# Kernel optimization log

Hardware: AMD Instinct MI355X
Metric: run time of the kernel (lower is better)

The kernel has to match this reference:

```python
import jax, jax.numpy as jnp
import numpy as np

D_MODEL = 1024
DFF = 4096
SPARSITY = 0.5
EPS = 1e-6


def layer_norm(x, gamma, beta):
    mu = jnp.mean(x, axis=-1, keepdims=True)
    var = jnp.mean(jnp.square(x - mu), axis=-1, keepdims=True)
    return (x - mu) * jax.lax.rsqrt(var + EPS) * gamma + beta


def setup_inputs() -> dict:
    key = jax.random.key(0)
    ks = jax.random.split(key, 8)
    B, S, d, f = 4, 2048, D_MODEL, DFF
    s = 1.0 / np.sqrt(d)
    return {
        "x": jax.random.normal(ks[0], (B, S, d), dtype=jnp.float32),
        "Wq": jax.random.normal(ks[1], (d, d), dtype=jnp.float32) * s,
        "bq": jnp.zeros((d,), jnp.float32),
        "Wk": jax.random.normal(ks[2], (d, d), dtype=jnp.float32) * s,
        "bk": jnp.zeros((d,), jnp.float32),
        "Wv": jax.random.normal(ks[3], (d, d), dtype=jnp.float32) * s,
        "bv": jnp.zeros((d,), jnp.float32),
        "W1": jax.random.normal(ks[4], (d, f), dtype=jnp.float32) * s,
        "b1": jnp.zeros((f,), jnp.float32),
        "W2": jax.random.normal(ks[5], (f, d), dtype=jnp.float32) * (1.0 / np.sqrt(f)),
        "b2": jnp.zeros((d,), jnp.float32),
        "gamma1": jnp.ones((d,), jnp.float32),
        "beta1": jnp.zeros((d,), jnp.float32),
        "gamma2": jnp.ones((d,), jnp.float32),
        "beta2": jnp.zeros((d,), jnp.float32),
    }


def reference(x, Wq, bq, Wk, bk, Wv, bv, W1, b1, W2, b2, gamma1, beta1, gamma2, beta2):
    B, S, d = x.shape
    q = x @ Wq + bq
    k = x @ Wk + bk
    v = x @ Wv + bv
    # scores: [B, S, S], scaled by sqrt(d_model)
    scores = jnp.einsum("bqd,bkd->bqk", q, k) / jnp.sqrt(jnp.float32(d))
    # top-k sparsification: keep scores >= row-wise k-th largest, else 0
    topk = int(SPARSITY * S)
    top_vals = jax.lax.top_k(scores, topk)[0]  # sorted descending
    threshold = top_vals[..., -1:]
    sparse_scores = jnp.where(scores >= threshold, scores, jnp.zeros_like(scores))
    attn = jax.nn.softmax(sparse_scores, axis=-1)
    attn_out = jnp.einsum("bqk,bkd->bqd", attn, v)
    out1 = layer_norm(x + attn_out, gamma1, beta1)
    ffn = jax.nn.relu(out1 @ W1 + b1) @ W2 + b2
    return layer_norm(out1 + ffn, gamma2, beta2)
```

## Files before the change

kernel.cpp:

```cpp
#include <hip/hip_runtime.h>
#include <cstdint>

typedef unsigned short u16;
typedef __attribute__((ext_vector_type(8))) short s16x8;
typedef __attribute__((ext_vector_type(4))) unsigned short u16x4;
typedef __attribute__((ext_vector_type(4))) float f32x4;

__device__ __forceinline__ u16 f2bf(float f) {
  union { float f; uint32_t u; } c; c.f = f;
  uint32_t r = c.u + 0x7FFFu + ((c.u >> 16) & 1u);
  return (u16)(r >> 16);
}
__device__ __forceinline__ float wave_sum_f(float v) {
#pragma unroll
  for (int o = 32; o > 0; o >>= 1) v += __shfl_xor(v, o);
  return v;
}
__device__ __forceinline__ float wave_max_f(float v) {
#pragma unroll
  for (int o = 32; o > 0; o >>= 1) v = fmaxf(v, __shfl_xor(v, o));
  return v;
}
__device__ __forceinline__ void gload16(const u16* g, u16* l) {
  __builtin_amdgcn_global_load_lds(
      (const __attribute__((address_space(1))) unsigned int*)g,
      (__attribute__((address_space(3))) unsigned int*)l,
      16, 0, 0);
}

__global__ __launch_bounds__(256)
void cast_f32_bf16(const float* __restrict__ in, u16* __restrict__ out) {
  long i = ((long)blockIdx.x * 256 + threadIdx.x) * 4;
  f32x4 v = *(const f32x4*)(in + i);
  u16x4 o;
#pragma unroll
  for (int j = 0; j < 4; ++j) o[j] = f2bf(v[j]);
  *(u16x4*)(out + i) = o;
}

__global__ __launch_bounds__(256)
void concat3(const float* __restrict__ a, const float* __restrict__ b,
             const float* __restrict__ c, float* __restrict__ o) {
  int i = blockIdx.x * 256 + threadIdx.x;
  o[i] = i < 1024 ? a[i] : (i < 2048 ? b[i - 1024] : c[i - 2048]);
}

__global__ __launch_bounds__(256)
void transpose_cast_f32_bf16(const float* __restrict__ in, u16* __restrict__ out,
                             int R, int C) {
  __shared__ float tile[32][33];
  int r0 = blockIdx.y * 32, c0 = blockIdx.x * 32;
  int tid = threadIdx.x;
  int tr = tid >> 3, tc4 = (tid & 7) * 4;
  f32x4 v = *(const f32x4*)(in + (long)(r0 + tr) * C + c0 + tc4);
#pragma unroll
  for (int j = 0; j < 4; ++j) tile[tr][tc4 + j] = v[j];
  __syncthreads();
  u16x4 o;
#pragma unroll
  for (int j = 0; j < 4; ++j) o[j] = f2bf(tile[tc4 + j][tr]);
  *(u16x4*)(out + (long)(c0 + tr) * R + r0 + tc4) = o;
}

__global__ __launch_bounds__(256)
void transpose_bf16(const u16* __restrict__ in, u16* __restrict__ out,
                    int R, int C, int in_rs, long in_batch, long out_batch) {
  __shared__ u16 tile[32][36];
  const long zin = (long)blockIdx.z * in_batch;
  const long zout = (long)blockIdx.z * out_batch;
  int r0 = blockIdx.y * 32, c0 = blockIdx.x * 32;
  int tid = threadIdx.x;
  int tr = tid >> 3, tc4 = (tid & 7) * 4;
  u16x4 v = *(const u16x4*)(in + zin + (long)(r0 + tr) * in_rs + c0 + tc4);
#pragma unroll
  for (int j = 0; j < 4; ++j) tile[tr][tc4 + j] = v[j];
  __syncthreads();
  u16x4 o;
#pragma unroll
  for (int j = 0; j < 4; ++j) o[j] = tile[tc4 + j][tr];
  *(u16x4*)(out + zout + (long)(c0 + tr) * R + r0 + tc4) = o;
}

#define TBM 256
#define TBK 64

enum { EPI_BF16_BIAS = 0, EPI_F32_SCALE = 1, EPI_F32 = 2,
       EPI_RELU_BF16_BIAS = 3, EPI_F32_BIAS_RESID = 4 };

#define QUAD(MFA)                                                             \
  _Pragma("unroll")                                                           \
  for (int mf = (MFA); mf < (MFA) + 2; ++mf)                                  \
    _Pragma("unroll")                                                         \
    for (int nf = 0; nf < 4; ++nf) {                                          \
      acc[mf][nf] = __builtin_amdgcn_mfma_f32_16x16x32_bf16(                  \
          af[mf][0], bfr[nf][0], acc[mf][nf], 0, 0, 0);                       \
      acc[mf][nf] = __builtin_amdgcn_mfma_f32_16x16x32_bf16(                  \
          af[mf][1], bfr[nf][1], acc[mf][nf], 0, 0, 0);                       \
    }

template <int BN_, int EPI>
__global__ __launch_bounds__(512, 2)
void gemm8p(const u16* __restrict__ A, const u16* __restrict__ Bt,
            const float* __restrict__ bias, const float* __restrict__ resid,
            void* __restrict__ Cout, int M, int N, int K, int lda, int ldb,
            int tx, int ty, long long batchA, long long batchB, long long batchC,
            float scale) {
  constexpr int MF = (BN_ == 256) ? 8 : 4;
  constexpr int NBI = BN_ / 128;
  __shared__ u16 As[2][TBM * TBK];
  __shared__ u16 Bs[2][BN_ * TBK];

  const int nwg = gridDim.x;
  const int orig = blockIdx.x;
  const int q = nwg >> 3, r = nwg & 7;
  const int xcd = orig & 7, idx = orig >> 3;
  const int wg = (xcd < r ? xcd * (q + 1) : r * (q + 1) + (xcd - r) * q) + idx;
  const int bx = wg % tx;
  const int tmp = wg / tx;
  const int by = tmp % ty;
  const int b  = tmp / ty;

  const u16* Ab = A + (long)b * batchA;
  const u16* Bb = Bt + (long)b * batchB;
  const int row0 = by * TBM;
  const int col0 = bx * BN_;
  const int tid = threadIdx.x;
  const int lane = tid & 63, wid = tid >> 6;
  const int wm = (BN_ == 256) ? (wid >> 2) : (wid >> 1);
  const int wn = (BN_ == 256) ? (wid & 3) : (wid & 1);
  const int rowW = (BN_ == 256) ? wm * 128 : wm * 64;
  const int l15 = lane & 15, g = lane >> 4;

  const int sr = lane >> 3;
  const int sc = ((lane & 7) ^ sr) * 8;
  const int wrow = wid * 8 + sr;

  const int c0 = ((0 + g) ^ (l15 & 7)) * 8;
  const int c1 = ((4 + g) ^ (l15 & 7)) * 8;

  auto stageA = [&](int h, int kt, int bf_) {
#pragma unroll
    for (int j = 0; j < 2; ++j)
      gload16(Ab + (size_t)(row0 + h * 128 + j * 64 + wrow) * lda + kt * TBK + sc,
              &As[bf_][(h * 128 + j * 64 + wid * 8) * TBK]);
  };
  auto stageB = [&](int h, int kt, int bf_) {
#pragma unroll
    for (int j = 0; j < NBI; ++j)
      gload16(Bb + (size_t)(col0 + h * (BN_ / 2) + j * 64 + wrow) * ldb + kt * TBK + sc,
              &Bs[bf_][(h * (BN_ / 2) + j * 64 + wid * 8) * TBK]);
  };

  s16x8 af[MF][2];
  s16x8 bfr[4][2];
  f32x4 acc[MF][4] = {};
  const int nt = K / TBK;

  stageA(0, 0, 0); stageA(1, 0, 0);
  stageB(0, 0, 0); stageB(1, 0, 0);
  if (nt > 1) {
    stageA(0, 1, 1); stageA(1, 1, 1);
    asm volatile("s_waitcnt vmcnt(4)" ::: "memory");
  } else {
    asm volatile("s_waitcnt vmcnt(0)" ::: "memory");
  }
  __builtin_amdgcn_s_barrier();

  for (int t = 0; t < nt; ++t) {
    const int cur = t & 1;
    const u16* Asc = &As[cur][0];
    const u16* Bsc = &Bs[cur][0];

    if constexpr (BN_ == 256) {
#pragma unroll
      for (int nf = 0; nf < 4; ++nf) {
        const int rb = (wn * 64 + nf * 16 + l15) * TBK;
        bfr[nf][0] = *(const s16x8*)(Bsc + rb + c0);
        bfr[nf][1] = *(const s16x8*)(Bsc + rb + c1);
      }
#pragma unroll
      for (int mf = 0; mf < 4; ++mf) {
        const int rb = (rowW + mf * 16 + l15) * TBK;
        af[mf][0] = *(const s16x8*)(Asc + rb + c0);
        af[mf][1] = *(const s16x8*)(Asc + rb + c1);
      }
      if (t + 1 < nt) stageB(0, t + 1, cur ^ 1);
      __builtin_amdgcn_s_barrier();
      __builtin_amdgcn_s_setprio(1);
      QUAD(0)
      __builtin_amdgcn_s_setprio(0);
      __builtin_amdgcn_s_barrier();

#pragma unroll
      for (int mf = 4; mf < 8; ++mf) {
        const int rb = (rowW + mf * 16 + l15) * TBK;
        af[mf][0] = *(const s16x8*)(Asc + rb + c0);
        af[mf][1] = *(const s16x8*)(Asc + rb + c1);
      }
      if (t + 1 < nt) stageB(1, t + 1, cur ^ 1);
      __builtin_amdgcn_s_barrier();
      __builtin_amdgcn_s_setprio(1);
      QUAD(2)
      __builtin_amdgcn_s_setprio(0);
      asm volatile("s_waitcnt lgkmcnt(0)" ::: "memory");
      __builtin_amdgcn_sched_barrier(0);
      __builtin_amdgcn_s_barrier();

      if (t + 2 < nt) stageA(0, t + 2, cur);
      __builtin_amdgcn_s_barrier();
      __builtin_amdgcn_s_setprio(1);
      QUAD(4)
      __builtin_amdgcn_s_setprio(0);
      __builtin_amdgcn_s_barrier();

      if (t + 2 < nt) stageA(1, t + 2, cur);
      __builtin_amdgcn_s_barrier();
      __builtin_amdgcn_s_setprio(1);
      QUAD(6)
      __builtin_amdgcn_s_setprio(0);
      if (t + 1 < nt) {
        if (t + 2 < nt) asm volatile("s_waitcnt vmcnt(4)" ::: "memory");
        else            asm volatile("s_waitcnt vmcnt(0)" ::: "memory");
      }
      __builtin_amdgcn_s_barrier();
    } else {
#pragma unroll
      for (int nf = 0; nf < 4; ++nf) {
        const int rb = (wn * 64 + nf * 16 + l15) * TBK;
        bfr[nf][0] = *(const s16x8*)(Bsc + rb + c0);
        bfr[nf][1] = *(const s16x8*)(Bsc + rb + c1);
      }
#pragma unroll
      for (int mf = 0; mf < 4; ++mf) {
        const int rb = (rowW + mf * 16 + l15) * TBK;
        af[mf][0] = *(const s16x8*)(Asc + rb + c0);
        af[mf][1] = *(const s16x8*)(Asc + rb + c1);
      }
      if (t + 1 < nt) { stageB(0, t + 1, cur ^ 1); stageB(1, t + 1, cur ^ 1); }
      asm volatile("s_waitcnt lgkmcnt(0)" ::: "memory");
      __builtin_amdgcn_sched_barrier(0);
      __builtin_amdgcn_s_barrier();
      __builtin_amdgcn_s_setprio(1);
      QUAD(0)
      __builtin_amdgcn_s_setprio(0);
      if (t + 2 < nt) { stageA(0, t + 2, cur); stageA(1, t + 2, cur); }
      __builtin_amdgcn_s_setprio(1);
      QUAD(2)
      __builtin_amdgcn_s_setprio(0);
      if (t + 1 < nt) {
        if (t + 2 < nt) asm volatile("s_waitcnt vmcnt(4)" ::: "memory");
        else            asm volatile("s_waitcnt vmcnt(0)" ::: "memory");
        __builtin_amdgcn_s_barrier();
      }
    }
  }

  const long cb = (long)b * batchC;
#pragma unroll
  for (int mf = 0; mf < MF; ++mf) {
    const int rbase = row0 + rowW + mf * 16 + g * 4;
#pragma unroll
    for (int nf = 0; nf < 4; ++nf) {
      const int col = col0 + wn * 64 + nf * 16 + l15;
#pragma unroll
      for (int rr = 0; rr < 4; ++rr) {
        const long cidx = cb + (long)(rbase + rr) * N + col;
        float v = acc[mf][nf][rr];
        if (EPI == EPI_BF16_BIAS) {
          ((u16*)Cout)[cidx] = f2bf(v + bias[col]);
        } else if (EPI == EPI_F32_SCALE) {
          ((float*)Cout)[cidx] = v * scale;
        } else if (EPI == EPI_F32) {
          ((float*)Cout)[cidx] = v;
        } else if (EPI == EPI_RELU_BF16_BIAS) {
          ((u16*)Cout)[cidx] = f2bf(fmaxf(v + bias[col], 0.0f));
        } else {
          ((float*)Cout)[cidx] = v + bias[col] + resid[cidx];
        }
      }
    }
  }
}

__global__ __launch_bounds__(256)
void topk_softmax(const float* __restrict__ scores, u16* __restrict__ P, int topk) {
  const int lane = threadIdx.x & 63, wid = threadIdx.x >> 6;
  const long row = (long)blockIdx.x * 4 + wid;
  const long rowoff = row * 2048;

  float v[32]; uint32_t kv[32];
  const float2* src = (const float2*)(scores + rowoff);
#pragma unroll
  for (int j = 0; j < 16; ++j) {
    float2 f = src[j * 64 + lane];
    v[2 * j] = f.x; v[2 * j + 1] = f.y;
  }
#pragma unroll
  for (int j = 0; j < 32; ++j) {
    union { float f; uint32_t u; } c; c.f = v[j];
    kv[j] = (c.u & 0x80000000u) ? ~c.u : (c.u | 0x80000000u);
  }
  float m = v[0];
#pragma unroll
  for (int j = 1; j < 32; ++j) m = fmaxf(m, v[j]);
  m = wave_max_f(m);

  uint32_t cur = 0;
  for (int bit = 31; bit >= 0; --bit) {
    const uint32_t cand = cur | (1u << bit);
    int c = 0;
#pragma unroll
    for (int j = 0; j < 32; ++j)
      c += (int)__popcll(__ballot(kv[j] >= cand));
    if (c >= topk) cur = cand;
  }

  const float mm = fmaxf(m, 0.0f);
  float p[32], s = 0.0f;
#pragma unroll
  for (int j = 0; j < 32; ++j) {
    float val = (kv[j] >= cur) ? v[j] : 0.0f;
    p[j] = __expf(val - mm);
    s += p[j];
  }
  s = wave_sum_f(s);
  const float inv = 1.0f / s;
  uint32_t* dst = (uint32_t*)(P + rowoff);
#pragma unroll
  for (int j = 0; j < 16; ++j) {
    uint32_t w = (uint32_t)f2bf(p[2 * j] * inv) |
                 ((uint32_t)f2bf(p[2 * j + 1] * inv) << 16);
    dst[j * 64 + lane] = w;
  }
}

__global__ __launch_bounds__(256)
void add_ln(const float* __restrict__ a, const float* __restrict__ r,
            const float* __restrict__ gamma, const float* __restrict__ beta,
            float* __restrict__ outf, u16* __restrict__ outb) {
  const long off = (long)blockIdx.x * 1024;
  const int tid = threadIdx.x, lane = tid & 63, wid = tid >> 6;
  __shared__ float sred[4];
  float x[4];
#pragma unroll
  for (int j = 0; j < 4; ++j) {
    int col = j * 256 + tid;
    float t = a[off + col];
    if (r) t += r[off + col];
    x[j] = t;
  }
  float s = x[0] + x[1] + x[2] + x[3];
  s = wave_sum_f(s);
  if (lane == 0) sred[wid] = s;
  __syncthreads();
  float mu = (sred[0] + sred[1] + sred[2] + sred[3]) * (1.0f / 1024.0f);
  __syncthreads();
  float qv = 0.0f;
#pragma unroll
  for (int j = 0; j < 4; ++j) { float d = x[j] - mu; qv += d * d; }
  qv = wave_sum_f(qv);
  if (lane == 0) sred[wid] = qv;
  __syncthreads();
  float var = (sred[0] + sred[1] + sred[2] + sred[3]) * (1.0f / 1024.0f);
  float inv = rsqrtf(var + 1e-6f);
#pragma unroll
  for (int j = 0; j < 4; ++j) {
    int col = j * 256 + tid;
    float o = (x[j] - mu) * inv * gamma[col] + beta[col];
    if (outf) outf[off + col] = o;
    if (outb) outb[off + col] = f2bf(o);
  }
}

extern "C" void kernel_launch(void* const* d_in, const int* in_sizes, int n_in,
                              void* d_out, int out_size, void* d_ws, size_t ws_size,
                              hipStream_t stream) {
  const float* x   = (const float*)d_in[0];
  const float* Wq  = (const float*)d_in[1];
  const float* bq  = (const float*)d_in[2];
  const float* Wk  = (const float*)d_in[3];
  const float* bk  = (const float*)d_in[4];
  const float* Wv  = (const float*)d_in[5];
  const float* bv  = (const float*)d_in[6];
  const float* W1  = (const float*)d_in[7];
  const float* b1  = (const float*)d_in[8];
  const float* W2  = (const float*)d_in[9];
  const float* b2  = (const float*)d_in[10];
  const float* g1  = (const float*)d_in[11];
  const float* be1 = (const float*)d_in[12];
  const float* g2  = (const float*)d_in[13];
  const float* be2 = (const float*)d_in[14];

  const int Bz = 4, S = 2048, Dm = 1024, Ff = 4096;
  const int M = Bz * S;
  const int N3 = 3 * Dm;

  char* ws = (char*)d_ws;
  const size_t MBy = 1024u * 1024u;
  u16*  wqkvT  = (u16*)(ws + 0 * MBy);
  u16*  w1T    = (u16*)(ws + 6 * MBy);
  u16*  w2T    = (u16*)(ws + 14 * MBy);
  u16*  xbf    = (u16*)(ws + 23 * MBy);
  u16*  qkv    = (u16*)(ws + 39 * MBy);
  u16*  vT     = (u16*)(ws + 87 * MBy);
  float* bqkv  = (float*)(ws + 103 * MBy);
  float* scores= (float*)(ws + 103 * MBy);
  u16*  P      = (u16*)(ws + 167 * MBy);
  float* attn  = (float*)(ws + 103 * MBy);
  float* out1  = (float*)(ws + 135 * MBy);
  u16*  out1b  = (u16*)(ws + 23 * MBy);
  u16*  hbf    = (u16*)(ws + 39 * MBy);
  float* y     = (float*)(ws + 167 * MBy);

  dim3 blk(256);
  dim3 blk8(512);

  cast_f32_bf16<<<dim3((unsigned)((long)M * Dm / 1024)), blk, 0, stream>>>(x, xbf);
  transpose_cast_f32_bf16<<<dim3(Dm / 32, Dm / 32), blk, 0, stream>>>(Wq, wqkvT, Dm, Dm);
  transpose_cast_f32_bf16<<<dim3(Dm / 32, Dm / 32), blk, 0, stream>>>(Wk, wqkvT + 1024 * 1024, Dm, Dm);
  transpose_cast_f32_bf16<<<dim3(Dm / 32, Dm / 32), blk, 0, stream>>>(Wv, wqkvT + 2048 * 1024, Dm, Dm);
  transpose_cast_f32_bf16<<<dim3(Ff / 32, Dm / 32), blk, 0, stream>>>(W1, w1T, Dm, Ff);
  transpose_cast_f32_bf16<<<dim3(Dm / 32, Ff / 32), blk, 0, stream>>>(W2, w2T, Ff, Dm);
  concat3<<<dim3(12), blk, 0, stream>>>(bq, bk, bv, bqkv);

  gemm8p<128, EPI_BF16_BIAS><<<dim3(24 * 32), blk8, 0, stream>>>(
      xbf, wqkvT, bqkv, nullptr, qkv, M, N3, Dm, Dm, Dm, 24, 32, 0, 0, 0, 1.0f);

  transpose_bf16<<<dim3(Dm / 32, S / 32, Bz), blk, 0, stream>>>(
      qkv + 2048, vT, S, Dm, N3, (long)S * N3, (long)Dm * S);

  gemm8p<256, EPI_F32_SCALE><<<dim3(8 * 8 * Bz), blk8, 0, stream>>>(
      qkv, qkv + 1024, nullptr, nullptr, scores, S, S, Dm, N3, N3, 8, 8,
      (long long)S * N3, (long long)S * N3, (long long)S * S, 0.03125f);

  topk_softmax<<<dim3(Bz * S / 4), blk, 0, stream>>>(scores, P, S / 2);

  gemm8p<128, EPI_F32><<<dim3(8 * 8 * Bz), blk8, 0, stream>>>(
      P, vT, nullptr, nullptr, attn, S, Dm, S, S, S, 8, 8,
      (long long)S * S, (long long)Dm * S, (long long)S * Dm, 1.0f);

  add_ln<<<dim3(M), blk, 0, stream>>>(x, attn, g1, be1, out1, out1b);

  gemm8p<256, EPI_RELU_BF16_BIAS><<<dim3(16 * 32), blk8, 0, stream>>>(
      out1b, w1T, b1, nullptr, hbf, M, Ff, Dm, Dm, Dm, 16, 32, 0, 0, 0, 1.0f);

  gemm8p<128, EPI_F32_BIAS_RESID><<<dim3(8 * 32), blk8, 0, stream>>>(
      hbf, w2T, b2, out1, y, M, Dm, Ff, Ff, Ff, 8, 32, 0, 0, 0, 1.0f);

  add_ln<<<dim3(M), blk, 0, stream>>>(y, nullptr, g2, be2, (float*)d_out, nullptr);
}
```

Measured before the change: 404.7 us.

## Store attention scores in bf16 and unify GEMM prefetch pipeline at distance two

The QK^T GEMM epilogue now writes scaled scores as bf16 instead of fp32, and topk_softmax reads them back as bf16. This halves the write and read traffic of the large B×S×S score tensor. Separately, the GEMM main loop drops the four-phase BN=256 schedule in favor of one loop that prefetches both A and B two tiles ahead, with fewer barriers. The bf16 scores lose precision, so the top-k threshold can see more ties and keep a different set of entries, and the new overlap schedule may hide memory latency differently.

After: 408.7 us. About the same (+1.0%).

```diff
diff --git a/kernel.cpp b/kernel.cpp
--- a/kernel.cpp
+++ b/kernel.cpp
@@ -10,6 +10,10 @@
   union { float f; uint32_t u; } c; c.f = f;
   uint32_t r = c.u + 0x7FFFu + ((c.u >> 16) & 1u);
   return (u16)(r >> 16);
+}
+__device__ __forceinline__ float bf2f(u16 b) {
+  union { uint32_t u; float f; } c; c.u = ((uint32_t)b) << 16;
+  return c.f;
 }
 __device__ __forceinline__ float wave_sum_f(float v) {
 #pragma unroll
@@ -84,7 +88,7 @@
 #define TBM 256
 #define TBK 64
 
-enum { EPI_BF16_BIAS = 0, EPI_F32_SCALE = 1, EPI_F32 = 2,
+enum { EPI_BF16_BIAS = 0, EPI_BF16_SCALE = 1, EPI_F32 = 2,
        EPI_RELU_BF16_BIAS = 3, EPI_F32_BIAS_RESID = 4 };
 
 #define QUAD(MFA)                                                             \
@@ -100,7 +104,7 @@
 
 template <int BN_, int EPI>
 __global__ __launch_bounds__(512, 2)
-void gemm8p(const u16* __restrict__ A, const u16* __restrict__ Bt,
+void gemm2p(const u16* __restrict__ A, const u16* __restrict__ Bt,
             const float* __restrict__ bias, const float* __restrict__ resid,
             void* __restrict__ Cout, int M, int N, int K, int lda, int ldb,
             int tx, int ty, long long batchA, long long batchB, long long batchC,
@@ -160,7 +164,9 @@
   stageB(0, 0, 0); stageB(1, 0, 0);
   if (nt > 1) {
     stageA(0, 1, 1); stageA(1, 1, 1);
-    asm volatile("s_waitcnt vmcnt(4)" ::: "memory");
+    stageB(0, 1, 1); stageB(1, 1, 1);
+    if constexpr (BN_ == 256) asm volatile("s_waitcnt vmcnt(8)" ::: "memory");
+    else                      asm volatile("s_waitcnt vmcnt(6)" ::: "memory");
   } else {
     asm volatile("s_waitcnt vmcnt(0)" ::: "memory");
   }
@@ -171,87 +177,41 @@
     const u16* Asc = &As[cur][0];
     const u16* Bsc = &Bs[cur][0];
 
-    if constexpr (BN_ == 256) {
-#pragma unroll
-      for (int nf = 0; nf < 4; ++nf) {
-        const int rb = (wn * 64 + nf * 16 + l15) * TBK;
-        bfr[nf][0] = *(const s16x8*)(Bsc + rb + c0);
-        bfr[nf][1] = *(const s16x8*)(Bsc + rb + c1);
-      }
-#pragma unroll
-      for (int mf = 0; mf < 4; ++mf) {
-        const int rb = (rowW + mf * 16 + l15) * TBK;
-        af[mf][0] = *(const s16x8*)(Asc + rb + c0);
-        af[mf][1] = *(const s16x8*)(Asc + rb + c1);
-      }
-      if (t + 1 < nt) stageB(0, t + 1, cur ^ 1);
-      __builtin_amdgcn_s_barrier();
-      __builtin_amdgcn_s_setprio(1);
-      QUAD(0)
-      __builtin_amdgcn_s_setprio(0);
-      __builtin_amdgcn_s_barrier();
-
-#pragma unroll
-      for (int mf = 4; mf < 8; ++mf) {
-        const int rb = (rowW + mf * 16 + l15) * TBK;
-        af[mf][0] = *(const s16x8*)(Asc + rb + c0);
-        af[mf][1] = *(const s16x8*)(Asc + rb + c1);
-      }
-      if (t + 1 < nt) stageB(1, t + 1, cur ^ 1);
-      __builtin_amdgcn_s_barrier();
-      __builtin_amdgcn_s_setprio(1);
-      QUAD(2)
-      __builtin_amdgcn_s_setprio(0);
-      asm volatile("s_waitcnt lgkmcnt(0)" ::: "memory");
-      __builtin_amdgcn_sched_barrier(0);
-      __builtin_amdgcn_s_barrier();
-
-      if (t + 2 < nt) stageA(0, t + 2, cur);
-      __builtin_amdgcn_s_barrier();
-      __builtin_amdgcn_s_setprio(1);
-      QUAD(4)
-      __builtin_amdgcn_s_setprio(0);
-      __builtin_amdgcn_s_barrier();
-
-      if (t + 2 < nt) stageA(1, t + 2, cur);
-      __builtin_amdgcn_s_barrier();
-      __builtin_amdgcn_s_setprio(1);
-      QUAD(6)
-      __builtin_amdgcn_s_setprio(0);
-      if (t + 1 < nt) {
-        if (t + 2 < nt) asm volatile("s_waitcnt vmcnt(4)" ::: "memory");
-        else            asm volatile("s_waitcnt vmcnt(0)" ::: "memory");
+#pragma unroll
+    for (int nf = 0; nf < 4; ++nf) {
+      const int rb = (wn * 64 + nf * 16 + l15) * TBK;
+      bfr[nf][0] = *(const s16x8*)(Bsc + rb + c0);
+      bfr[nf][1] = *(const s16x8*)(Bsc + rb + c1);
+    }
+#pragma unroll
+    for (int mf = 0; mf < MF; ++mf) {
+      const int rb = (rowW + mf * 16 + l15) * TBK;
+      af[mf][0] = *(const s16x8*)(Asc + rb + c0);
+      af[mf][1] = *(const s16x8*)(Asc + rb + c1);
+    }
+    asm volatile("s_waitcnt lgkmcnt(0)" ::: "memory");
+    __builtin_amdgcn_sched_barrier(0);
+    __builtin_amdgcn_s_barrier();
+
+    if (t + 2 < nt) { stageB(0, t + 2, cur); stageB(1, t + 2, cur); }
+    __builtin_amdgcn_s_setprio(1);
+    QUAD(0)
+    if constexpr (MF == 8) { QUAD(2) }
+    __builtin_amdgcn_s_setprio(0);
+    if (t + 2 < nt) { stageA(0, t + 2, cur); stageA(1, t + 2, cur); }
+    __builtin_amdgcn_s_setprio(1);
+    if constexpr (MF == 8) { QUAD(4) QUAD(6) }
+    else                   { QUAD(2) }
+    __builtin_amdgcn_s_setprio(0);
+
+    if (t + 1 < nt) {
+      if (t + 2 < nt) {
+        if constexpr (BN_ == 256) asm volatile("s_waitcnt vmcnt(8)" ::: "memory");
+        else                      asm volatile("s_waitcnt vmcnt(6)" ::: "memory");
+      } else {
+        asm volatile("s_waitcnt vmcnt(0)" ::: "memory");
       }
       __builtin_amdgcn_s_barrier();
-    } else {
-#pragma unroll
-      for (int nf = 0; nf < 4; ++nf) {
-        const int rb = (wn * 64 + nf * 16 + l15) * TBK;
-        bfr[nf][0] = *(const s16x8*)(Bsc + rb + c0);
-        bfr[nf][1] = *(const s16x8*)(Bsc + rb + c1);
-      }
-#pragma unroll
-      for (int mf = 0; mf < 4; ++mf) {
-        const int rb = (rowW + mf * 16 + l15) * TBK;
-        af[mf][0] = *(const s16x8*)(Asc + rb + c0);
-        af[mf][1] = *(const s16x8*)(Asc + rb + c1);
-      }
-      if (t + 1 < nt) { stageB(0, t + 1, cur ^ 1); stageB(1, t + 1, cur ^ 1); }
-      asm volatile("s_waitcnt lgkmcnt(0)" ::: "memory");
-      __builtin_amdgcn_sched_barrier(0);
-      __builtin_amdgcn_s_barrier();
-      __builtin_amdgcn_s_setprio(1);
-      QUAD(0)
-      __builtin_amdgcn_s_setprio(0);
-      if (t + 2 < nt) { stageA(0, t + 2, cur); stageA(1, t + 2, cur); }
-      __builtin_amdgcn_s_setprio(1);
-      QUAD(2)
-      __builtin_amdgcn_s_setprio(0);
-      if (t + 1 < nt) {
-        if (t + 2 < nt) asm volatile("s_waitcnt vmcnt(4)" ::: "memory");
-        else            asm volatile("s_waitcnt vmcnt(0)" ::: "memory");
-        __builtin_amdgcn_s_barrier();
-      }
     }
   }
 
@@ -268,8 +228,8 @@
         float v = acc[mf][nf][rr];
         if (EPI == EPI_BF16_BIAS) {
           ((u16*)Cout)[cidx] = f2bf(v + bias[col]);
-        } else if (EPI == EPI_F32_SCALE) {
-          ((float*)Cout)[cidx] = v * scale;
+        } else if (EPI == EPI_BF16_SCALE) {
+          ((u16*)Cout)[cidx] = f2bf(v * scale);
         } else if (EPI == EPI_F32) {
           ((float*)Cout)[cidx] = v;
         } else if (EPI == EPI_RELU_BF16_BIAS) {
@@ -283,17 +243,18 @@
 }
 
 __global__ __launch_bounds__(256)
-void topk_softmax(const float* __restrict__ scores, u16* __restrict__ P, int topk) {
+void topk_softmax(const u16* __restrict__ scores, u16* __restrict__ P, int topk) {
   const int lane = threadIdx.x & 63, wid = threadIdx.x >> 6;
   const long row = (long)blockIdx.x * 4 + wid;
   const long rowoff = row * 2048;
 
   float v[32]; uint32_t kv[32];
-  const float2* src = (const float2*)(scores + rowoff);
+  const uint32_t* src = (const uint32_t*)(scores + rowoff);
 #pragma unroll
   for (int j = 0; j < 16; ++j) {
-    float2 f = src[j * 64 + lane];
-    v[2 * j] = f.x; v[2 * j + 1] = f.y;
+    uint32_t w = src[j * 64 + lane];
+    v[2 * j]     = bf2f((u16)(w & 0xFFFFu));
+    v[2 * j + 1] = bf2f((u16)(w >> 16));
   }
 #pragma unroll
   for (int j = 0; j < 32; ++j) {
@@ -404,7 +365,7 @@
   u16*  qkv    = (u16*)(ws + 39 * MBy);
   u16*  vT     = (u16*)(ws + 87 * MBy);
   float* bqkv  = (float*)(ws + 103 * MBy);
-  float* scores= (float*)(ws + 103 * MBy);
+  u16*  scores = (u16*)(ws + 103 * MBy);
   u16*  P      = (u16*)(ws + 167 * MBy);
   float* attn  = (float*)(ws + 103 * MBy);
   float* out1  = (float*)(ws + 135 * MBy);
@@ -423,28 +384,28 @@
   transpose_cast_f32_bf16<<<dim3(Dm / 32, Ff / 32), blk, 0, stream>>>(W2, w2T, Ff, Dm);
   concat3<<<dim3(12), blk, 0, stream>>>(bq, bk, bv, bqkv);
 
-  gemm8p<128, EPI_BF16_BIAS><<<dim3(24 * 32), blk8, 0, stream>>>(
+  gemm2p<128, EPI_BF16_BIAS><<<dim3(24 * 32), blk8, 0, stream>>>(
       xbf, wqkvT, bqkv, nullptr, qkv, M, N3, Dm, Dm, Dm, 24, 32, 0, 0, 0, 1.0f);
 
   transpose_bf16<<<dim3(Dm / 32, S / 32, Bz), blk, 0, stream>>>(
       qkv + 2048, vT, S, Dm, N3, (long)S * N3, (long)Dm * S);
 
-  gemm8p<256, EPI_F32_SCALE><<<dim3(8 * 8 * Bz), blk8, 0, stream>>>(
+  gemm2p<256, EPI_BF16_SCALE><<<dim3(8 * 8 * Bz), blk8, 0, stream>>>(
       qkv, qkv + 1024, nullptr, nullptr, scores, S, S, Dm, N3, N3, 8, 8,
       (long long)S * N3, (long long)S * N3, (long long)S * S, 0.03125f);
 
   topk_softmax<<<dim3(Bz * S / 4), blk, 0, stream>>>(scores, P, S / 2);
 
-  gemm8p<128, EPI_F32><<<dim3(8 * 8 * Bz), blk8, 0, stream>>>(
+  gemm2p<128, EPI_F32><<<dim3(8 * 8 * Bz), blk8, 0, stream>>>(
       P, vT, nullptr, nullptr, attn, S, Dm, S, S, S, 8, 8,
       (long long)S * S, (long long)Dm * S, (long long)S * Dm, 1.0f);
 
   add_ln<<<dim3(M), blk, 0, stream>>>(x, attn, g1, be1, out1, out1b);
 
-  gemm8p<256, EPI_RELU_BF16_BIAS><<<dim3(16 * 32), blk8, 0, stream>>>(
+  gemm2p<256, EPI_RELU_BF16_BIAS><<<dim3(16 * 32), blk8, 0, stream>>>(
       out1b, w1T, b1, nullptr, hbf, M, Ff, Dm, Dm, Dm, 16, 32, 0, 0, 0, 1.0f);
 
-  gemm8p<128, EPI_F32_BIAS_RESID><<<dim3(8 * 32), blk8, 0, stream>>>(
+  gemm2p<128, EPI_F32_BIAS_RESID><<<dim3(8 * 32), blk8, 0, stream>>>(
       hbf, w2T, b2, out1, y, M, Dm, Ff, Ff, Ff, 8, 32, 0, 0, 0, 1.0f);
 
   add_ln<<<dim3(M), blk, 0, stream>>>(y, nullptr, g2, be2, (float*)d_out, nullptr);
```

## Store scores, attention output and residual as bf16 to cut memory traffic

Applied to the files above, without the earlier changes.

Stores the QK^T scores, the attention output and the post-LN residual in bf16 instead of fp32. The final FFN GEMM now reads the bf16 out1 as its residual, and add_ln is vectorised to use 4-wide loads and stores. This roughly halves the traffic of the 64MB scores buffer and the other intermediates. In exchange, top-k thresholding on bf16 scores produces ties and rounding, so the selected set can differ from the reference, and the residual path loses precision.

After: 383.9 us. -5.1%, faster.

```diff
diff --git a/kernel.cpp b/kernel.cpp
--- a/kernel.cpp
+++ b/kernel.cpp
@@ -10,6 +10,10 @@
   union { float f; uint32_t u; } c; c.f = f;
   uint32_t r = c.u + 0x7FFFu + ((c.u >> 16) & 1u);
   return (u16)(r >> 16);
+}
+__device__ __forceinline__ float bf2f(u16 b) {
+  union { uint32_t u; float f; } c; c.u = ((uint32_t)b) << 16;
+  return c.f;
 }
 __device__ __forceinline__ float wave_sum_f(float v) {
 #pragma unroll
@@ -84,8 +88,8 @@
 #define TBM 256
 #define TBK 64
 
-enum { EPI_BF16_BIAS = 0, EPI_F32_SCALE = 1, EPI_F32 = 2,
-       EPI_RELU_BF16_BIAS = 3, EPI_F32_BIAS_RESID = 4 };
+enum { EPI_BF16_BIAS = 0, EPI_BF16_SCALE = 1, EPI_BF16 = 2,
+       EPI_RELU_BF16_BIAS = 3, EPI_F32_BIAS_RESIDBF = 4 };
 
 #define QUAD(MFA)                                                             \
   _Pragma("unroll")                                                           \
@@ -101,7 +105,7 @@
 template <int BN_, int EPI>
 __global__ __launch_bounds__(512, 2)
 void gemm8p(const u16* __restrict__ A, const u16* __restrict__ Bt,
-            const float* __restrict__ bias, const float* __restrict__ resid,
+            const float* __restrict__ bias, const u16* __restrict__ resid,
             void* __restrict__ Cout, int M, int N, int K, int lda, int ldb,
             int tx, int ty, long long batchA, long long batchB, long long batchC,
             float scale) {
@@ -268,14 +272,14 @@
         float v = acc[mf][nf][rr];
         if (EPI == EPI_BF16_BIAS) {
           ((u16*)Cout)[cidx] = f2bf(v + bias[col]);
-        } else if (EPI == EPI_F32_SCALE) {
-          ((float*)Cout)[cidx] = v * scale;
-        } else if (EPI == EPI_F32) {
-          ((float*)Cout)[cidx] = v;
+        } else if (EPI == EPI_BF16_SCALE) {
+          ((u16*)Cout)[cidx] = f2bf(v * scale);
+        } else if (EPI == EPI_BF16) {
+          ((u16*)Cout)[cidx] = f2bf(v);
         } else if (EPI == EPI_RELU_BF16_BIAS) {
           ((u16*)Cout)[cidx] = f2bf(fmaxf(v + bias[col], 0.0f));
         } else {
-          ((float*)Cout)[cidx] = v + bias[col] + resid[cidx];
+          ((float*)Cout)[cidx] = v + bias[col] + bf2f(resid[cidx]);
         }
       }
     }
@@ -283,17 +287,18 @@
 }
 
 __global__ __launch_bounds__(256)
-void topk_softmax(const float* __restrict__ scores, u16* __restrict__ P, int topk) {
+void topk_softmax(const u16* __restrict__ scores, u16* __restrict__ P, int topk) {
   const int lane = threadIdx.x & 63, wid = threadIdx.x >> 6;
   const long row = (long)blockIdx.x * 4 + wid;
   const long rowoff = row * 2048;
 
   float v[32]; uint32_t kv[32];
-  const float2* src = (const float2*)(scores + rowoff);
+  const uint32_t* src = (const uint32_t*)(scores + rowoff);
 #pragma unroll
   for (int j = 0; j < 16; ++j) {
-    float2 f = src[j * 64 + lane];
-    v[2 * j] = f.x; v[2 * j + 1] = f.y;
+    uint32_t w = src[j * 64 + lane];
+    v[2 * j]     = bf2f((u16)(w & 0xFFFFu));
+    v[2 * j + 1] = bf2f((u16)(w >> 16));
   }
 #pragma unroll
   for (int j = 0; j < 32; ++j) {
@@ -335,19 +340,22 @@
 }
 
 __global__ __launch_bounds__(256)
-void add_ln(const float* __restrict__ a, const float* __restrict__ r,
+void add_ln(const float* __restrict__ a, const u16* __restrict__ r,
             const float* __restrict__ gamma, const float* __restrict__ beta,
             float* __restrict__ outf, u16* __restrict__ outb) {
   const long off = (long)blockIdx.x * 1024;
   const int tid = threadIdx.x, lane = tid & 63, wid = tid >> 6;
+  const int c4 = tid * 4;
   __shared__ float sred[4];
   float x[4];
-#pragma unroll
-  for (int j = 0; j < 4; ++j) {
-    int col = j * 256 + tid;
-    float t = a[off + col];
-    if (r) t += r[off + col];
-    x[j] = t;
+  f32x4 av = *(const f32x4*)(a + off + c4);
+  if (r) {
+    u16x4 rv = *(const u16x4*)(r + off + c4);
+#pragma unroll
+    for (int j = 0; j < 4; ++j) x[j] = av[j] + bf2f(rv[j]);
+  } else {
+#pragma unroll
+    for (int j = 0; j < 4; ++j) x[j] = av[j];
   }
   float s = x[0] + x[1] + x[2] + x[3];
   s = wave_sum_f(s);
@@ -363,13 +371,16 @@
   __syncthreads();
   float var = (sred[0] + sred[1] + sred[2] + sred[3]) * (1.0f / 1024.0f);
   float inv = rsqrtf(var + 1e-6f);
+  f32x4 gv = *(const f32x4*)(gamma + c4);
+  f32x4 bv = *(const f32x4*)(beta + c4);
+  f32x4 ov; u16x4 ob;
 #pragma unroll
   for (int j = 0; j < 4; ++j) {
-    int col = j * 256 + tid;
-    float o = (x[j] - mu) * inv * gamma[col] + beta[col];
-    if (outf) outf[off + col] = o;
-    if (outb) outb[off + col] = f2bf(o);
-  }
+    float o = (x[j] - mu) * inv * gv[j] + bv[j];
+    ov[j] = o; ob[j] = f2bf(o);
+  }
+  if (outf) *(f32x4*)(outf + off + c4) = ov;
+  if (outb) *(u16x4*)(outb + off + c4) = ob;
 }
 
 extern "C" void kernel_launch(void* const* d_in, const int* in_sizes, int n_in,
@@ -404,10 +415,9 @@
   u16*  qkv    = (u16*)(ws + 39 * MBy);
   u16*  vT     = (u16*)(ws + 87 * MBy);
   float* bqkv  = (float*)(ws + 103 * MBy);
-  float* scores= (float*)(ws + 103 * MBy);
+  u16*  scores = (u16*)(ws + 103 * MBy);
   u16*  P      = (u16*)(ws + 167 * MBy);
-  float* attn  = (float*)(ws + 103 * MBy);
-  float* out1  = (float*)(ws + 135 * MBy);
+  u16*  attn   = (u16*)(ws + 135 * MBy);
   u16*  out1b  = (u16*)(ws + 23 * MBy);
   u16*  hbf    = (u16*)(ws + 39 * MBy);
   float* y     = (float*)(ws + 167 * MBy);
@@ -429,23 +439,23 @@
   transpose_bf16<<<dim3(Dm / 32, S / 32, Bz), blk, 0, stream>>>(
       qkv + 2048, vT, S, Dm, N3, (long)S * N3, (long)Dm * S);
 
-  gemm8p<256, EPI_F32_SCALE><<<dim3(8 * 8 * Bz), blk8, 0, stream>>>(
+  gemm8p<256, EPI_BF16_SCALE><<<dim3(8 * 8 * Bz), blk8, 0, stream>>>(
       qkv, qkv + 1024, nullptr, nullptr, scores, S, S, Dm, N3, N3, 8, 8,
       (long long)S * N3, (long long)S * N3, (long long)S * S, 0.03125f);
 
   topk_softmax<<<dim3(Bz * S / 4), blk, 0, stream>>>(scores, P, S / 2);
 
-  gemm8p<128, EPI_F32><<<dim3(8 * 8 * Bz), blk8, 0, stream>>>(
+  gemm8p<128, EPI_BF16><<<dim3(8 * 8 * Bz), blk8, 0, stream>>>(
       P, vT, nullptr, nullptr, attn, S, Dm, S, S, S, 8, 8,
       (long long)S * S, (long long)Dm * S, (long long)S * Dm, 1.0f);
 
-  add_ln<<<dim3(M), blk, 0, stream>>>(x, attn, g1, be1, out1, out1b);
+  add_ln<<<dim3(M), blk, 0, stream>>>(x, attn, g1, be1, nullptr, out1b);
 
   gemm8p<256, EPI_RELU_BF16_BIAS><<<dim3(16 * 32), blk8, 0, stream>>>(
       out1b, w1T, b1, nullptr, hbf, M, Ff, Dm, Dm, Dm, 16, 32, 0, 0, 0, 1.0f);
 
-  gemm8p<128, EPI_F32_BIAS_RESID><<<dim3(8 * 32), blk8, 0, stream>>>(
-      hbf, w2T, b2, out1, y, M, Dm, Ff, Ff, Ff, 8, 32, 0, 0, 0, 1.0f);
+  gemm8p<128, EPI_F32_BIAS_RESIDBF><<<dim3(8 * 32), blk8, 0, stream>>>(
+      hbf, w2T, b2, out1b, y, M, Dm, Ff, Ff, Ff, 8, 32, 0, 0, 0, 1.0f);
 
   add_ln<<<dim3(M), blk, 0, stream>>>(y, nullptr, g2, be2, (float*)d_out, nullptr);
 }
```
